# Kernel optimization log

Measured on AMD Instinct MI355X. Metric: run time of the kernel, lower is better.

## Reference

```python
import jax, jax.numpy as jnp
import numpy as np

PADDING = 1
STRIDE = 1


def setup_inputs() -> dict:
    key = jax.random.key(0)
    k1, k2 = jax.random.split(key)
    x = jax.random.normal(k1, (3, 2048, 2048), dtype=jnp.float32)
    kernel = jax.random.normal(k2, (16, 3, 3, 3), dtype=jnp.float32) * 0.1
    return {"x": x, "kernel": kernel}


def reference(x, kernel):
    # x: [C, H, W], kernel: [OC, IC, kh, kw]
    # Equivalent to the naive loop conv with zero padding=1, stride=1, no bias.
    out = jax.lax.conv_general_dilated(
        x[None],                      # [1, C, H, W]
        kernel,                       # [OC, IC, kh, kw]
        window_strides=(STRIDE, STRIDE),
        padding=[(PADDING, PADDING), (PADDING, PADDING)],
        dimension_numbers=("NCHW", "OIHW", "NCHW"),
    )
    return out[0]                     # [OC, H_out, W_out]
```

## Files before the change

### kernel.cpp

```cpp
#include <hip/hip_runtime.h>


#define CONV_H 2048
#define CONV_W 2048
#define CONV_IC 3
#define CONV_OC 16

__global__ void conv_weight_transpose(const float* __restrict__ k,
                                      float* __restrict__ wt) {
    int t = threadIdx.x;
    if (t < CONV_OC * CONV_IC * 9) {
        int oc = t / 27;
        int r  = t % 27;
        wt[r * CONV_OC + oc] = k[t];
    }
}

__global__ __launch_bounds__(256) void conv2d_main(const float* __restrict__ x,
                                                   const float* __restrict__ wt,
                                                   float* __restrict__ out) {
    const int tid = blockIdx.x * 256 + threadIdx.x;
    const int w4  = tid & (CONV_W / 4 - 1);
    const int h   = tid >> 9;
    const int w0  = w4 << 2;

    float acc[CONV_OC][4];
#pragma unroll
    for (int oc = 0; oc < CONV_OC; ++oc)
#pragma unroll
        for (int j = 0; j < 4; ++j) acc[oc][j] = 0.f;

#pragma unroll
    for (int ic = 0; ic < CONV_IC; ++ic) {
        const float* plane = x + (size_t)ic * CONV_H * CONV_W;
#pragma unroll
        for (int kh = 0; kh < 3; ++kh) {
            const int hy = h + kh - 1;
            if (hy >= 0 && hy < CONV_H) {
                const float* row = plane + (size_t)hy * CONV_W;
                float in[6];
                const float4 c = *reinterpret_cast<const float4*>(row + w0);
                in[0] = (w0 > 0) ? row[w0 - 1] : 0.f;
                in[1] = c.x; in[2] = c.y; in[3] = c.z; in[4] = c.w;
                in[5] = (w0 + 4 < CONV_W) ? row[w0 + 4] : 0.f;
#pragma unroll
                for (int kw = 0; kw < 3; ++kw) {
                    const float* wp = wt + ((ic * 3 + kh) * 3 + kw) * CONV_OC;
#pragma unroll
                    for (int oc = 0; oc < CONV_OC; ++oc) {
                        const float wv = wp[oc];
#pragma unroll
                        for (int j = 0; j < 4; ++j)
                            acc[oc][j] = fmaf(in[kw + j], wv, acc[oc][j]);
                    }
                }
            }
        }
    }

    float* obase = out + (size_t)h * CONV_W + w0;
#pragma unroll
    for (int oc = 0; oc < CONV_OC; ++oc) {
        float4 v = make_float4(acc[oc][0], acc[oc][1], acc[oc][2], acc[oc][3]);
        *reinterpret_cast<float4*>(obase + (size_t)oc * CONV_H * CONV_W) = v;
    }
}

extern "C" void kernel_launch(void* const* d_in, const int* in_sizes, int n_in,
                              void* d_out, int out_size, void* d_ws, size_t ws_size,
                              hipStream_t stream) {
    const float* x = (const float*)d_in[0];
    const float* k = (const float*)d_in[1];
    float* out = (float*)d_out;
    float* wt  = (float*)d_ws;

    conv_weight_transpose<<<1, 512, 0, stream>>>(k, wt);

    const int total_threads = CONV_H * (CONV_W / 4);
    conv2d_main<<<total_threads / 256, 256, 0, stream>>>(x, wt, out);
}
```

Measured before the change: 326.6 us.

## Swizzle block order across XCDs, batch row loads, use nontemporal stores

Remaps block indices with (b&7)*512+(b>>3) so that consecutive row blocks run on the same XCD and can share halo rows in L2. Moves each input channel's three row loads ahead of the FMA loop and turns the channel loop into a non-unrolled one, keeping code size and register use in check. Output stores become nontemporal so the large write stream does not evict input lines from cache. This risks a different load/compute schedule and less latency hiding from the rolled loop.

```diff
diff --git a/kernel.cpp b/kernel.cpp
--- a/kernel.cpp
+++ b/kernel.cpp
@@ -3,56 +3,64 @@
 
 #define CONV_H 2048
 #define CONV_W 2048
-#define CONV_IC 3
-#define CONV_OC 16
+
+typedef float f32x4 __attribute__((ext_vector_type(4)));
 
 __global__ void conv_weight_transpose(const float* __restrict__ k,
                                       float* __restrict__ wt) {
     int t = threadIdx.x;
-    if (t < CONV_OC * CONV_IC * 9) {
+    if (t < 16 * 27) {
         int oc = t / 27;
         int r  = t % 27;
-        wt[r * CONV_OC + oc] = k[t];
+        wt[r * 16 + oc] = k[t];
     }
 }
 
 __global__ __launch_bounds__(256) void conv2d_main(const float* __restrict__ x,
                                                    const float* __restrict__ wt,
                                                    float* __restrict__ out) {
-    const int tid = blockIdx.x * 256 + threadIdx.x;
-    const int w4  = tid & (CONV_W / 4 - 1);
-    const int h   = tid >> 9;
-    const int w0  = w4 << 2;
+    int b = (int)blockIdx.x;
+    b = (b & 7) * 512 + (b >> 3);
 
-    float acc[CONV_OC][4];
+    const int h  = b >> 1;
+    const int w0 = ((b & 1) * 256 + (int)threadIdx.x) << 2;
+
+    float acc[16][4];
 #pragma unroll
-    for (int oc = 0; oc < CONV_OC; ++oc)
+    for (int oc = 0; oc < 16; ++oc)
 #pragma unroll
         for (int j = 0; j < 4; ++j) acc[oc][j] = 0.f;
 
-#pragma unroll
-    for (int ic = 0; ic < CONV_IC; ++ic) {
-        const float* plane = x + (size_t)ic * CONV_H * CONV_W;
+#pragma unroll 1
+    for (int ic = 0; ic < 3; ++ic) {
+        const float* plane = x + (size_t)ic * (CONV_H * CONV_W);
+        float in[3][6];
 #pragma unroll
         for (int kh = 0; kh < 3; ++kh) {
             const int hy = h + kh - 1;
             if (hy >= 0 && hy < CONV_H) {
                 const float* row = plane + (size_t)hy * CONV_W;
-                float in[6];
-                const float4 c = *reinterpret_cast<const float4*>(row + w0);
-                in[0] = (w0 > 0) ? row[w0 - 1] : 0.f;
-                in[1] = c.x; in[2] = c.y; in[3] = c.z; in[4] = c.w;
-                in[5] = (w0 + 4 < CONV_W) ? row[w0 + 4] : 0.f;
+                const f32x4 c = *reinterpret_cast<const f32x4*>(row + w0);
+                in[kh][0] = (w0 > 0) ? row[w0 - 1] : 0.f;
+                in[kh][1] = c.x; in[kh][2] = c.y;
+                in[kh][3] = c.z; in[kh][4] = c.w;
+                in[kh][5] = (w0 + 4 < CONV_W) ? row[w0 + 4] : 0.f;
+            } else {
 #pragma unroll
-                for (int kw = 0; kw < 3; ++kw) {
-                    const float* wp = wt + ((ic * 3 + kh) * 3 + kw) * CONV_OC;
+                for (int j = 0; j < 6; ++j) in[kh][j] = 0.f;
+            }
+        }
 #pragma unroll
-                    for (int oc = 0; oc < CONV_OC; ++oc) {
-                        const float wv = wp[oc];
+        for (int kh = 0; kh < 3; ++kh) {
 #pragma unroll
-                        for (int j = 0; j < 4; ++j)
-                            acc[oc][j] = fmaf(in[kw + j], wv, acc[oc][j]);
-                    }
+            for (int kw = 0; kw < 3; ++kw) {
+                const float* wp = wt + ((ic * 3 + kh) * 3 + kw) * 16;
+#pragma unroll
+                for (int oc = 0; oc < 16; ++oc) {
+                    const float wv = wp[oc];
+#pragma unroll
+                    for (int j = 0; j < 4; ++j)
+                        acc[oc][j] = fmaf(in[kh][kw + j], wv, acc[oc][j]);
                 }
             }
         }
@@ -60,9 +68,10 @@
 
     float* obase = out + (size_t)h * CONV_W + w0;
 #pragma unroll
-    for (int oc = 0; oc < CONV_OC; ++oc) {
-        float4 v = make_float4(acc[oc][0], acc[oc][1], acc[oc][2], acc[oc][3]);
-        *reinterpret_cast<float4*>(obase + (size_t)oc * CONV_H * CONV_W) = v;
+    for (int oc = 0; oc < 16; ++oc) {
+        f32x4 v = { acc[oc][0], acc[oc][1], acc[oc][2], acc[oc][3] };
+        __builtin_nontemporal_store(
+            v, reinterpret_cast<f32x4*>(obase + (size_t)oc * (CONV_H * CONV_W)));
     }
 }
 
@@ -76,6 +85,5 @@
 
     conv_weight_transpose<<<1, 512, 0, stream>>>(k, wt);
 
-    const int total_threads = CONV_H * (CONV_W / 4);
-    conv2d_main<<<total_threads / 256, 256, 0, stream>>>(x, wt, out);
+    conv2d_main<<<4096, 256, 0, stream>>>(x, wt, out);
 }
```

Result: faster. 319.5 us (-2.2%).
